# Performance work log

Hardware: AMD Instinct MI355X
Metric: run time of the kernel (lower is better)

The kernel has to match this reference:

```python
import jax, jax.numpy as jnp
import numpy as np

EPS = 1e-8  # matches torch F.cosine_similarity default eps


def _flatten_spatial(x):
    # [B, C, d, h, w] -> [B, N, C]
    B, C = x.shape[:2]
    return x.reshape(B, C, -1).transpose(0, 2, 1)


def _stage_loss(canon_src, canon_tgt, src_desc, tgt_desc):
    stage_size = src_desc.shape[2:]
    B, C = canon_src.shape[:2]
    # trilinear resize with half-pixel centers == torch align_corners=False
    rs = jax.image.resize(canon_src, (B, C) + stage_size, method='trilinear')
    rt = jax.image.resize(canon_tgt, (B, C) + stage_size, method='trilinear')
    a = _flatten_spatial(rs)  # [B, N, 3]
    b = _flatten_spatial(rt)  # [B, N, 3]
    # squared euclidean distances (argmin is invariant to sqrt)
    a2 = jnp.sum(a * a, axis=-1)  # [B, N]
    b2 = jnp.sum(b * b, axis=-1)  # [B, N]
    ab = jnp.einsum('bnc,bmc->bnm', a, b)  # [B, N, N]
    d2 = a2[:, :, None] + b2[:, None, :] - 2.0 * ab
    nearest = jnp.argmin(d2, axis=-1)  # [B, N] int
    sd = _flatten_spatial(src_desc)  # [B, N, Cd]
    td = _flatten_spatial(tgt_desc)  # [B, N, Cd]
    gathered = jnp.take_along_axis(td, nearest[:, :, None], axis=1)  # [B, N, Cd]
    num = jnp.sum(sd * gathered, axis=-1)
    denom = jnp.maximum(jnp.linalg.norm(sd, axis=-1), EPS) * \
            jnp.maximum(jnp.linalg.norm(gathered, axis=-1), EPS)
    cos = num / denom
    return 1.0 - jnp.mean(cos)


def setup_inputs() -> dict:
    key = jax.random.key(0)
    ks = jax.random.split(key, 6)
    return {
        'canonical_source': jax.random.normal(ks[0], (4, 3, 64, 64, 64), jnp.float32),
        'canonical_target': jax.random.normal(ks[1], (4, 3, 64, 64, 64), jnp.float32),
        'src_desc0': jax.random.normal(ks[2], (4, 32, 16, 16, 16), jnp.float32),
        'tgt_desc0': jax.random.normal(ks[3], (4, 32, 16, 16, 16), jnp.float32),
        'src_desc1': jax.random.normal(ks[4], (4, 32, 8, 8, 8), jnp.float32),
        'tgt_desc1': jax.random.normal(ks[5], (4, 32, 8, 8, 8), jnp.float32),
    }


def reference(canonical_source, canonical_target, src_desc0, tgt_desc0, src_desc1, tgt_desc1):
    l0 = _stage_loss(canonical_source, canonical_target, src_desc0, tgt_desc0)
    l1 = _stage_loss(canonical_source, canonical_target, src_desc1, tgt_desc1)
    return jnp.stack([l0, l1]).mean()
```

## Files before the change

### kernel.cpp

```cpp
#include <hip/hip_runtime.h>
#include <cfloat>

typedef unsigned long long u64;

#define CDESC 32
#define N0 4096
#define N1 512

__device__ __forceinline__ unsigned fbits_mono(float d) {
    unsigned b = __float_as_uint(d);
    return (d >= 0.f) ? (b | 0x80000000u) : ~b;
}

__device__ __forceinline__ void wave_reduce_atomic(float v, float* acc) {
#pragma unroll
    for (int off = 32; off > 0; off >>= 1) v += __shfl_down(v, off, 64);
    if ((threadIdx.x & 63) == 0) atomicAdd(acc, v);
}

__global__ __launch_bounds__(256) void pass1_fused(
        const float* __restrict__ csrc, const float* __restrict__ ctgt,
        const float* __restrict__ sd0, const float* __restrict__ td0,
        const float* __restrict__ sd1, const float* __restrict__ td1,
        float* __restrict__ t16a, float* __restrict__ t16b,
        float* __restrict__ t8a,  float* __restrict__ t8b,
        float* __restrict__ sd0T, float* __restrict__ td0T,
        float* __restrict__ sd1T, float* __restrict__ td1T,
        float* __restrict__ acc) {
    __shared__ __align__(16) float sRow[4096];
    const int tid = threadIdx.x;
    const int bx  = blockIdx.x, by = blockIdx.y;
    if (by == 0 && bx == 0 && tid < 4) acc[tid] = 0.f;

    if (bx < 768) {
        int bc = bx >> 6, z = bx & 63;
        const float* in = by ? ctgt : csrc;
        float* o16 = by ? t16b : t16a;
        float* o8  = by ? t8b  : t8a;
        const float4* src = (const float4*)(in + (size_t)(bc * 64 + z) * 4096);
        float4* dst = (float4*)sRow;
#pragma unroll
        for (int k = 0; k < 4; ++k)
            dst[tid + k * 256] = src[tid + k * 256];
        __syncthreads();
#pragma unroll
        for (int k = 0; k < 6; ++k) {
            int o = tid + k * 256;
            if (o < 1024) {
                int y = o >> 4, xo = o & 15;
                int j0 = 4 * xo - 2;
                float sum = 0.f, wsum = 0.f;
#pragma unroll
                for (int t = 0; t < 8; ++t) {
                    int j = j0 + t;
                    float w = 1.f - fabsf((float)t - 3.5f) / 4.f;
                    if (j >= 0 && j < 64) { sum = fmaf(w, sRow[y * 64 + j], sum); wsum += w; }
                }
                o16[bc * 65536 + z * 1024 + y * 16 + xo] = sum / wsum;
            } else {
                int o2 = o - 1024;
                int y = o2 >> 3, xo = o2 & 7;
                int j0 = 8 * xo - 4;
                float sum = 0.f, wsum = 0.f;
#pragma unroll
                for (int t = 0; t < 16; ++t) {
                    int j = j0 + t;
                    float w = 1.f - fabsf((float)t - 7.5f) / 8.f;
                    if (j >= 0 && j < 64) { sum = fmaf(w, sRow[y * 64 + j], sum); wsum += w; }
                }
                o8[bc * 32768 + z * 512 + y * 8 + xo] = sum / wsum;
            }
        }
    } else {
        __shared__ float tile[64 * 33];
        int tl = bx - 768;
        const float* din; float* dout; int N, b, n0;
        if (tl < 256) { din = by ? td0 : sd0; dout = by ? td0T : sd0T;
                        N = N0; b = tl >> 6; n0 = (tl & 63) * 64; }
        else { tl -= 256; din = by ? td1 : sd1; dout = by ? td1T : sd1T;
               N = N1; b = tl >> 3; n0 = (tl & 7) * 64; }
#pragma unroll
        for (int i = 0; i < 8; ++i) {
            int idx = tid + i * 256;
            int c = idx >> 6, j = idx & 63;
            tile[j * 33 + c] = din[((size_t)b * CDESC + c) * N + n0 + j];
        }
        __syncthreads();
#pragma unroll
        for (int i = 0; i < 8; ++i) {
            int idx = tid + i * 256;
            int p = idx >> 5, c = idx & 31;
            dout[((size_t)b * N + n0 + p) * CDESC + c] = tile[p * 33 + c];
        }
    }
}

__global__ __launch_bounds__(256) void pass2_both(
        const float* __restrict__ t16a, const float* __restrict__ t16b,
        const float* __restrict__ t8a,  const float* __restrict__ t8b,
        float4* __restrict__ ps0, float4* __restrict__ pt0,
        float4* __restrict__ ps1, float4* __restrict__ pt1) {
    int gid = blockIdx.x * 256 + threadIdx.x;
    if (blockIdx.x < 1024) {
        int sub = gid & 7, p = gid >> 3;
        int side = p >> 14, r = p & 16383;
        int b = r >> 12, n = r & 4095;
        int x = n & 15, y = (n >> 4) & 15, z = n >> 8;
        const float* t = side ? t16b : t16a;
        float wy[8]; int jy[8];
        float wys = 0.f, wzs = 0.f;
#pragma unroll
        for (int tt = 0; tt < 8; ++tt) {
            float w = 1.f - fabsf((float)tt - 3.5f) * 0.25f;
            int j = 4 * y - 2 + tt;
            bool v = (unsigned)j < 64u;
            wy[tt] = v ? w : 0.f; jy[tt] = v ? j : 0; wys += wy[tt];
            int jz = 4 * z - 2 + tt;
            if ((unsigned)jz < 64u) wzs += w;
        }
        float a0 = 0.f, a1 = 0.f, a2 = 0.f;
        {
            float wz = 1.f - fabsf((float)sub - 3.5f) * 0.25f;
            int jz = 4 * z - 2 + sub;
            if ((unsigned)jz < 64u) {
                const float* bz = t + (size_t)b * 196608 + jz * 1024 + x;
#pragma unroll
                for (int ty = 0; ty < 8; ++ty) {
                    float w = wz * wy[ty];
                    const float* pr = bz + jy[ty] * 16;
                    a0 = fmaf(w, pr[0],      a0);
                    a1 = fmaf(w, pr[65536],  a1);
                    a2 = fmaf(w, pr[131072], a2);
                }
            }
        }
#pragma unroll
        for (int m = 1; m < 8; m <<= 1) {
            a0 += __shfl_xor(a0, m, 64);
            a1 += __shfl_xor(a1, m, 64);
            a2 += __shfl_xor(a2, m, 64);
        }
        if (sub == 0) {
            float inv = 1.f / (wys * wzs);
            a0 *= inv; a1 *= inv; a2 *= inv;
            float4* pts = side ? pt0 : ps0;
            pts[b * N0 + n] = make_float4(a0, a1, a2, a0 * a0 + a1 * a1 + a2 * a2);
        }
    } else {
        int g = gid - 262144;
        int sub = g & 7, p = g >> 3;
        int side = p >> 11, r = p & 2047;
        int b = r >> 9, n = r & 511;
        int x = n & 7, y = (n >> 3) & 7, z = n >> 6;
        const float* t = side ? t8b : t8a;
        constexpr int CS = 64 * 64 * 8;
        float wy[16]; int jy[16];
        float wys = 0.f, wzs = 0.f;
#pragma unroll
        for (int tt = 0; tt < 16; ++tt) {
            float w = 1.f - fabsf((float)tt - 7.5f) * 0.125f;
            int j = 8 * y - 4 + tt;
            bool v = (unsigned)j < 64u;
            wy[tt] = v ? w : 0.f; jy[tt] = v ? j : 0; wys += wy[tt];
            int jz = 8 * z - 4 + tt;
            if ((unsigned)jz < 64u) wzs += w;
        }
        float a0 = 0.f, a1 = 0.f, a2 = 0.f;
#pragma unroll
        for (int k = 0; k < 2; ++k) {
            int tt = 2 * sub + k;
            float wz = 1.f - fabsf((float)tt - 7.5f) * 0.125f;
            int jz = 8 * z - 4 + tt;
            if ((unsigned)jz < 64u) {
                const float* bz = t + b * 3 * CS + jz * (64 * 8) + x;
#pragma unroll 1
                for (int ty = 0; ty < 16; ++ty) {
                    float w = wz * wy[ty];
                    const float* pr = bz + jy[ty] * 8;
                    a0 = fmaf(w, pr[0],      a0);
                    a1 = fmaf(w, pr[CS],     a1);
                    a2 = fmaf(w, pr[2 * CS], a2);
                }
            }
        }
#pragma unroll
        for (int m = 1; m < 8; m <<= 1) {
            a0 += __shfl_xor(a0, m, 64);
            a1 += __shfl_xor(a1, m, 64);
            a2 += __shfl_xor(a2, m, 64);
        }
        if (sub == 0) {
            float inv = 1.f / (wys * wzs);
            a0 *= inv; a1 *= inv; a2 *= inv;
            float4* pts = side ? pt1 : ps1;
            pts[b * N1 + n] = make_float4(a0, a1, a2, a0 * a0 + a1 * a1 + a2 * a2);
        }
    }
}

__device__ __forceinline__ float cos_pm(const float* __restrict__ sT,
                                        const float* __restrict__ tT,
                                        size_t si, size_t ti) {
    const float4* s = (const float4*)(sT + si * CDESC);
    const float4* t = (const float4*)(tT + ti * CDESC);
    float num = 0.f, s2 = 0.f, t2 = 0.f;
#pragma unroll
    for (int c = 0; c < 8; ++c) {
        float4 a = s[c], g = t[c];
        num = fmaf(a.x, g.x, fmaf(a.y, g.y, fmaf(a.z, g.z, fmaf(a.w, g.w, num))));
        s2  = fmaf(a.x, a.x, fmaf(a.y, a.y, fmaf(a.z, a.z, fmaf(a.w, a.w, s2))));
        t2  = fmaf(g.x, g.x, fmaf(g.y, g.y, fmaf(g.z, g.z, fmaf(g.w, g.w, t2))));
    }
    return num / (fmaxf(sqrtf(s2), 1e-8f) * fmaxf(sqrtf(t2), 1e-8f));
}

__global__ __launch_bounds__(256) void nn_cos_all(
        const float4* __restrict__ ps0, const float4* __restrict__ pt0,
        const float* __restrict__ sd0T, const float* __restrict__ td0T,
        const float4* __restrict__ ps1, const float4* __restrict__ pt1,
        const float* __restrict__ sd1T, const float* __restrict__ td1T,
        float* acc, float* __restrict__ out) {
    extern __shared__ __align__(16) char smraw[];
    float4* sm = (float4*)smraw;
    const int tid = threadIdx.x;
    const int bx  = blockIdx.x;

    if (bx < 256) {
        int b = bx >> 6, ptile = bx & 63;
        const float4* tp = pt0 + b * N0;
        for (int i = tid; i < N0; i += 256) {
            float4 q = tp[i];
            sm[i] = make_float4(-2.f * q.x, -2.f * q.y, -2.f * q.z, q.w);
        }
        __syncthreads();
        int w = tid >> 6, lane = tid & 63;
        int n = ptile * 64 + lane;
        float4 P = ps0[b * N0 + n];
        float best = FLT_MAX; int bi = 0;
        const int m0 = w * 1024;
#pragma unroll 16
        for (int k = 0; k < 1024; ++k) {
            float4 Q = sm[m0 + k];
            float d = fmaf(P.x, Q.x, fmaf(P.y, Q.y, fmaf(P.z, Q.z, Q.w)));
            if (d < best) { best = d; bi = k; }
        }
        u64 key = ((u64)fbits_mono(best) << 32) | (unsigned)(m0 + bi);
        __syncthreads();
        u64* keys = (u64*)smraw;
        keys[w * 64 + lane] = key;
        __syncthreads();
        if (tid < 64) {
            u64 k0 = keys[tid],       k1 = keys[tid + 64];
            u64 k2 = keys[tid + 128], k3 = keys[tid + 192];
            u64 ka = k0 < k1 ? k0 : k1;
            u64 kb = k2 < k3 ? k2 : k3;
            u64 kk = ka < kb ? ka : kb;
            int nearest = (int)(unsigned)(kk & 0xFFFFFFFFull);
            int n2 = ptile * 64 + tid;
            float cosv = cos_pm(sd0T, td0T, (size_t)b * N0 + n2,
                                (size_t)b * N0 + nearest);
            wave_reduce_atomic(cosv, acc + 0);
        }
    } else {
        int bb = bx - 256;
        int b = bb >> 1;
        const float4* tp = pt1 + b * N1;
        for (int i = tid; i < N1; i += 256) {
            float4 qq = tp[i];
            sm[i] = make_float4(-2.f * qq.x, -2.f * qq.y, -2.f * qq.z, qq.w);
        }
        __syncthreads();
        int n = (bb & 1) * 256 + tid;
        float4 P = ps1[b * N1 + n];
        float best = FLT_MAX; int bi = 0;
#pragma unroll 16
        for (int m = 0; m < N1; ++m) {
            float4 Q = sm[m];
            float d = fmaf(P.x, Q.x, fmaf(P.y, Q.y, fmaf(P.z, Q.z, Q.w)));
            if (d < best) { best = d; bi = m; }
        }
        float cosv = cos_pm(sd1T, td1T, (size_t)b * N1 + n, (size_t)b * N1 + bi);
        wave_reduce_atomic(cosv, acc + 1);
    }

    __syncthreads();
    if (tid == 0) {
        __threadfence();
        unsigned old = atomicAdd((unsigned*)(acc + 2), 1u);
        if (old == 263u) {
            float a0 = atomicAdd(acc + 0, 0.f);
            float a1 = atomicAdd(acc + 1, 0.f);
            out[0] = 1.f - 0.5f * (a0 * (1.f / 16384.f) + a1 * (1.f / 2048.f));
        }
    }
}

extern "C" void kernel_launch(void* const* d_in, const int* in_sizes, int n_in,
                              void* d_out, int out_size, void* d_ws, size_t ws_size,
                              hipStream_t stream) {
    const float* c_src = (const float*)d_in[0];
    const float* c_tgt = (const float*)d_in[1];
    const float* sd0   = (const float*)d_in[2];
    const float* td0   = (const float*)d_in[3];
    const float* sd1   = (const float*)d_in[4];
    const float* td1   = (const float*)d_in[5];
    float* out = (float*)d_out;

    char* ws = (char*)d_ws;
    float* acc  = (float*)ws;
    float* t16a = (float*)(ws + 256);
    float* t16b = t16a + 786432;
    float* t8a  = t16b + 786432;
    float* t8b  = t8a + 393216;
    float4* ps0 = (float4*)(t8b + 393216);
    float4* pt0 = ps0 + 16384;
    float4* ps1 = pt0 + 16384;
    float4* pt1 = ps1 + 2048;
    float* sd0T = (float*)(pt1 + 2048);
    float* td0T = sd0T + 524288;
    float* sd1T = td0T + 524288;
    float* td1T = sd1T + 65536;

    pass1_fused<<<dim3(1056, 2), 256, 0, stream>>>(c_src, c_tgt, sd0, td0, sd1, td1,
                                                   t16a, t16b, t8a, t8b,
                                                   sd0T, td0T, sd1T, td1T, acc);
    pass2_both<<<1152, 256, 0, stream>>>(t16a, t16b, t8a, t8b, ps0, pt0, ps1, pt1);
    nn_cos_all<<<264, 256, 65536, stream>>>(ps0, pt0, sd0T, td0T, ps1, pt1,
                                            sd1T, td1T, acc, out);
}
```

Measured before the change: 129.1 us.

## Split stage-0 NN search across block pairs with atomicMin merge and register blocking

```diff
diff --git a/kernel.cpp b/kernel.cpp
--- a/kernel.cpp
+++ b/kernel.cpp
@@ -26,11 +26,17 @@
         float* __restrict__ t8a,  float* __restrict__ t8b,
         float* __restrict__ sd0T, float* __restrict__ td0T,
         float* __restrict__ sd1T, float* __restrict__ td1T,
-        float* __restrict__ acc) {
+        float* __restrict__ acc, unsigned* __restrict__ tick,
+        u64* __restrict__ slot) {
     __shared__ __align__(16) float sRow[4096];
     const int tid = threadIdx.x;
     const int bx  = blockIdx.x, by = blockIdx.y;
-    if (by == 0 && bx == 0 && tid < 4) acc[tid] = 0.f;
+    if (by == 0) {
+        int gid = bx * 256 + tid;
+        if (gid < 4) acc[gid] = 0.f;
+        if (gid < 128) tick[gid] = 0u;
+        if (gid < 16384) slot[gid] = ~0ull;
+    }
 
     if (bx < 768) {
         int bc = bx >> 6, z = bx & 63;
@@ -219,44 +225,56 @@
         const float* __restrict__ sd0T, const float* __restrict__ td0T,
         const float4* __restrict__ ps1, const float4* __restrict__ pt1,
         const float* __restrict__ sd1T, const float* __restrict__ td1T,
-        float* acc, float* __restrict__ out) {
-    extern __shared__ __align__(16) char smraw[];
-    float4* sm = (float4*)smraw;
+        u64* slot, unsigned* tick, float* acc, float* __restrict__ out) {
+    __shared__ __align__(16) float4 sm[2048];
+    __shared__ u64 keys[512];
+    __shared__ int last_flag;
     const int tid = threadIdx.x;
     const int bx  = blockIdx.x;
+    const int w = tid >> 6, lane = tid & 63;
 
     if (bx < 256) {
-        int b = bx >> 6, ptile = bx & 63;
-        const float4* tp = pt0 + b * N0;
-        for (int i = tid; i < N0; i += 256) {
+        int b = bx >> 6, g = (bx >> 1) & 31, h = bx & 1;
+        const float4* tp = pt0 + b * N0 + h * 2048;
+        for (int i = tid; i < 2048; i += 256) {
             float4 q = tp[i];
             sm[i] = make_float4(-2.f * q.x, -2.f * q.y, -2.f * q.z, q.w);
         }
         __syncthreads();
-        int w = tid >> 6, lane = tid & 63;
-        int n = ptile * 64 + lane;
-        float4 P = ps0[b * N0 + n];
-        float best = FLT_MAX; int bi = 0;
-        const int m0 = w * 1024;
+        float4 P1 = ps0[b * N0 + g * 128 + lane];
+        float4 P2 = ps0[b * N0 + g * 128 + 64 + lane];
+        float b1 = FLT_MAX, b2 = FLT_MAX; int i1 = 0, i2 = 0;
+        const int m0 = w * 512;
 #pragma unroll 16
-        for (int k = 0; k < 1024; ++k) {
+        for (int k = 0; k < 512; ++k) {
             float4 Q = sm[m0 + k];
-            float d = fmaf(P.x, Q.x, fmaf(P.y, Q.y, fmaf(P.z, Q.z, Q.w)));
-            if (d < best) { best = d; bi = k; }
-        }
-        u64 key = ((u64)fbits_mono(best) << 32) | (unsigned)(m0 + bi);
-        __syncthreads();
-        u64* keys = (u64*)smraw;
-        keys[w * 64 + lane] = key;
-        __syncthreads();
-        if (tid < 64) {
-            u64 k0 = keys[tid],       k1 = keys[tid + 64];
-            u64 k2 = keys[tid + 128], k3 = keys[tid + 192];
+            float d1 = fmaf(P1.x, Q.x, fmaf(P1.y, Q.y, fmaf(P1.z, Q.z, Q.w)));
+            float d2 = fmaf(P2.x, Q.x, fmaf(P2.y, Q.y, fmaf(P2.z, Q.z, Q.w)));
+            if (d1 < b1) { b1 = d1; i1 = k; }
+            if (d2 < b2) { b2 = d2; i2 = k; }
+        }
+        unsigned mbase = (unsigned)(h * 2048 + m0);
+        keys[w * 64 + lane]       = ((u64)fbits_mono(b1) << 32) | (mbase + i1);
+        keys[256 + w * 64 + lane] = ((u64)fbits_mono(b2) << 32) | (mbase + i2);
+        __syncthreads();
+        if (tid < 128) {
+            int which = tid >> 6, l = tid & 63;
+            const u64* kp = keys + which * 256 + l;
+            u64 k0 = kp[0], k1 = kp[64], k2 = kp[128], k3 = kp[192];
             u64 ka = k0 < k1 ? k0 : k1;
             u64 kb = k2 < k3 ? k2 : k3;
-            u64 kk = ka < kb ? ka : kb;
+            atomicMin(&slot[b * N0 + g * 128 + which * 64 + l], ka < kb ? ka : kb);
+        }
+        __syncthreads();
+        if (tid == 0) {
+            __threadfence();
+            last_flag = (atomicAdd(&tick[b * 32 + g], 1u) == 1u);
+        }
+        __syncthreads();
+        if (last_flag && tid < 128) {
+            int n2 = g * 128 + tid;
+            u64 kk = atomicAdd(&slot[b * N0 + n2], 0ull);
             int nearest = (int)(unsigned)(kk & 0xFFFFFFFFull);
-            int n2 = ptile * 64 + tid;
             float cosv = cos_pm(sd0T, td0T, (size_t)b * N0 + n2,
                                 (size_t)b * N0 + nearest);
             wave_reduce_atomic(cosv, acc + 0);
@@ -307,8 +325,10 @@
     float* out = (float*)d_out;
 
     char* ws = (char*)d_ws;
-    float* acc  = (float*)ws;
-    float* t16a = (float*)(ws + 256);
+    float*    acc  = (float*)ws;
+    unsigned* tick = (unsigned*)(ws + 256);
+    u64*      slot = (u64*)(ws + 2048);
+    float* t16a = (float*)(ws + 2048 + 131072);
     float* t16b = t16a + 786432;
     float* t8a  = t16b + 786432;
     float* t8b  = t8a + 393216;
@@ -323,8 +343,9 @@
 
     pass1_fused<<<dim3(1056, 2), 256, 0, stream>>>(c_src, c_tgt, sd0, td0, sd1, td1,
                                                    t16a, t16b, t8a, t8b,
-                                                   sd0T, td0T, sd1T, td1T, acc);
+                                                   sd0T, td0T, sd1T, td1T,
+                                                   acc, tick, slot);
     pass2_both<<<1152, 256, 0, stream>>>(t16a, t16b, t8a, t8b, ps0, pt0, ps1, pt1);
-    nn_cos_all<<<264, 256, 65536, stream>>>(ps0, pt0, sd0T, td0T, ps1, pt1,
-                                            sd1T, td1T, acc, out);
-}
+    nn_cos_all<<<264, 256, 0, stream>>>(ps0, pt0, sd0T, td0T, ps1, pt1,
+                                        sd1T, td1T, slot, tick, acc, out);
+}
```

Measured after the change: 130.7 us. No clear change (+1.3%).

## Rotate stage-0 NN candidates through registers via DPP instead of LDS

Applied to the files above, without the earlier changes.

```diff
diff --git a/kernel.cpp b/kernel.cpp
--- a/kernel.cpp
+++ b/kernel.cpp
@@ -16,6 +16,13 @@
 #pragma unroll
     for (int off = 32; off > 0; off >>= 1) v += __shfl_down(v, off, 64);
     if ((threadIdx.x & 63) == 0) atomicAdd(acc, v);
+}
+
+__device__ __forceinline__ float dpp_rot1_f(float v) {
+    return __int_as_float(__builtin_amdgcn_mov_dpp(__float_as_int(v), 0x13C, 0xf, 0xf, 0));
+}
+__device__ __forceinline__ int dpp_rot1_i(int v) {
+    return __builtin_amdgcn_mov_dpp(v, 0x13C, 0xf, 0xf, 0);
 }
 
 __global__ __launch_bounds__(256) void pass1_fused(
@@ -220,34 +227,37 @@
         const float4* __restrict__ ps1, const float4* __restrict__ pt1,
         const float* __restrict__ sd1T, const float* __restrict__ td1T,
         float* acc, float* __restrict__ out) {
-    extern __shared__ __align__(16) char smraw[];
-    float4* sm = (float4*)smraw;
+    __shared__ u64 keys[256];
+    __shared__ __align__(16) float4 sm1[512];
     const int tid = threadIdx.x;
     const int bx  = blockIdx.x;
+    const int w = tid >> 6, lane = tid & 63;
 
     if (bx < 256) {
-        int b = bx >> 6, ptile = bx & 63;
-        const float4* tp = pt0 + b * N0;
-        for (int i = tid; i < N0; i += 256) {
-            float4 q = tp[i];
-            sm[i] = make_float4(-2.f * q.x, -2.f * q.y, -2.f * q.z, q.w);
-        }
-        __syncthreads();
-        int w = tid >> 6, lane = tid & 63;
-        int n = ptile * 64 + lane;
+        int b = bx >> 6, stile = bx & 63;
+        int n = stile * 64 + lane;
         float4 P = ps0[b * N0 + n];
-        float best = FLT_MAX; int bi = 0;
-        const int m0 = w * 1024;
-#pragma unroll 16
-        for (int k = 0; k < 1024; ++k) {
-            float4 Q = sm[m0 + k];
-            float d = fmaf(P.x, Q.x, fmaf(P.y, Q.y, fmaf(P.z, Q.z, Q.w)));
-            if (d < best) { best = d; bi = k; }
-        }
-        u64 key = ((u64)fbits_mono(best) << 32) | (unsigned)(m0 + bi);
-        __syncthreads();
-        u64* keys = (u64*)smraw;
-        keys[w * 64 + lane] = key;
+        float Px = -2.f * P.x, Py = -2.f * P.y, Pz = -2.f * P.z;
+        const float4* tq = pt0 + b * N0 + w * 1024;
+        float best = FLT_MAX; int bm = 0;
+        float4 T = tq[lane];
+        int idx = lane;
+#pragma unroll 1
+        for (int t = 0; t < 16; ++t) {
+            float4 Tn = tq[((t + 1) & 15) * 64 + lane];
+            float td_ = FLT_MAX; int ti_ = 0;
+#pragma unroll
+            for (int r = 0; r < 64; ++r) {
+                float d = fmaf(Px, T.x, fmaf(Py, T.y, fmaf(Pz, T.z, T.w)));
+                if (d < td_) { td_ = d; ti_ = idx; }
+                T.x = dpp_rot1_f(T.x); T.y = dpp_rot1_f(T.y);
+                T.z = dpp_rot1_f(T.z); T.w = dpp_rot1_f(T.w);
+                idx = dpp_rot1_i(idx);
+            }
+            if (td_ < best) { best = td_; bm = t * 64 + ti_; }
+            T = Tn;
+        }
+        keys[w * 64 + lane] = ((u64)fbits_mono(best) << 32) | (unsigned)(w * 1024 + bm);
         __syncthreads();
         if (tid < 64) {
             u64 k0 = keys[tid],       k1 = keys[tid + 64];
@@ -256,7 +266,7 @@
             u64 kb = k2 < k3 ? k2 : k3;
             u64 kk = ka < kb ? ka : kb;
             int nearest = (int)(unsigned)(kk & 0xFFFFFFFFull);
-            int n2 = ptile * 64 + tid;
+            int n2 = stile * 64 + tid;
             float cosv = cos_pm(sd0T, td0T, (size_t)b * N0 + n2,
                                 (size_t)b * N0 + nearest);
             wave_reduce_atomic(cosv, acc + 0);
@@ -267,7 +277,7 @@
         const float4* tp = pt1 + b * N1;
         for (int i = tid; i < N1; i += 256) {
             float4 qq = tp[i];
-            sm[i] = make_float4(-2.f * qq.x, -2.f * qq.y, -2.f * qq.z, qq.w);
+            sm1[i] = make_float4(-2.f * qq.x, -2.f * qq.y, -2.f * qq.z, qq.w);
         }
         __syncthreads();
         int n = (bb & 1) * 256 + tid;
@@ -275,7 +285,7 @@
         float best = FLT_MAX; int bi = 0;
 #pragma unroll 16
         for (int m = 0; m < N1; ++m) {
-            float4 Q = sm[m];
+            float4 Q = sm1[m];
             float d = fmaf(P.x, Q.x, fmaf(P.y, Q.y, fmaf(P.z, Q.z, Q.w)));
             if (d < best) { best = d; bi = m; }
         }
@@ -325,6 +335,6 @@
                                                    t16a, t16b, t8a, t8b,
                                                    sd0T, td0T, sd1T, td1T, acc);
     pass2_both<<<1152, 256, 0, stream>>>(t16a, t16b, t8a, t8b, ps0, pt0, ps1, pt1);
-    nn_cos_all<<<264, 256, 65536, stream>>>(ps0, pt0, sd0T, td0T, ps1, pt1,
-                                            sd1T, td1T, acc, out);
-}
+    nn_cos_all<<<264, 256, 0, stream>>>(ps0, pt0, sd0T, td0T, ps1, pt1,
+                                        sd1T, td1T, acc, out);
+}
```

New measurement: 131.2 us. No clear change (+1.6%).
